# Kernel tuning notes

Measured on AMD Instinct MI355X. Metric: run time of the kernel, lower is better.

Reference implementation:

```python
import jax, jax.numpy as jnp
import numpy as np

NUM_CLASSES = 80
NUM_ANCHORS = 3
IN_H, IN_W = 608, 608
GRID_H, GRID_W = 76, 76
BATCH = 16
# anchors selected by anchor_mask [0,1,2] out of the 9 COCO anchors
MASKED_ANCHORS = np.array([[10.0, 13.0], [16.0, 30.0], [33.0, 23.0]], dtype=np.float32)


def setup_inputs() -> dict:
    key = jax.random.key(0)
    x = jax.random.normal(key, (BATCH, NUM_ANCHORS * (5 + NUM_CLASSES), GRID_H, GRID_W), dtype=jnp.float32)
    anchors = jnp.asarray(MASKED_ANCHORS)
    return {"x": x, "anchors": anchors}


def reference(x, anchors):
    """YOLOv3 detection-layer forward (decode path of Yolo.__cal_bounding_box).

    x: [N, A*(5+C), H, W] raw conv output; anchors: [A, 2] (w, h) in pixels.
    Returns decoded predictions [N, A*H*W, 5+C] with normalized xywh boxes,
    objectness and class probabilities.
    """
    N, _, H, W = x.shape
    A, C = NUM_ANCHORS, NUM_CLASSES
    x = x.reshape(N, A, 5 + C, H, W)  # [N, A, 5+C, H, W]

    px = jax.nn.sigmoid(x[:, :, 0])            # [N, A, H, W]
    py = jax.nn.sigmoid(x[:, :, 1])
    pw = x[:, :, 2]
    ph = x[:, :, 3]
    conf = jax.nn.sigmoid(x[:, :, 4])          # [N, A, H, W]
    prob = jax.nn.sigmoid(x[:, :, 5:])         # [N, A, C, H, W]

    gy, gx = jnp.meshgrid(jnp.arange(H, dtype=x.dtype), jnp.arange(W, dtype=x.dtype), indexing="ij")
    # grid-offset decode, normalized to [0, 1] (matches __cal_bounding_box)
    bx = (px + gx) / W
    by = (py + gy) / H
    aw = anchors[:, 0].reshape(1, A, 1, 1)
    ah = anchors[:, 1].reshape(1, A, 1, 1)
    bw = jnp.exp(pw) * aw / IN_W
    bh = jnp.exp(ph) * ah / IN_H

    bbox = jnp.stack([bx, by, bw, bh, conf], axis=-1)      # [N, A, H, W, 5]
    prob = jnp.transpose(prob, (0, 1, 3, 4, 2))            # [N, A, H, W, C]
    out = jnp.concatenate([bbox, prob], axis=-1)           # [N, A, H, W, 5+C]
    return out.reshape(N, A * H * W, 5 + C)
```

## Files before the change

### kernel.cpp

```cpp
#include <hip/hip_runtime.h>
#include <math.h>


#define NCH     85
#define SPATIAL 5776
#define GWID    76
#define TS      64
#define NTILES  91

__device__ __forceinline__ float fast_sigmoid(float v) {
    return __builtin_amdgcn_rcpf(1.0f + __expf(-v));
}

__device__ __forceinline__ void process4(float* __restrict__ tile,
                                         int c, int sl, int s0,
                                         float4 v, float aw, float ah) {
    float vv[4] = {v.x, v.y, v.z, v.w};
    if (c >= 4) {
        #pragma unroll
        for (int jj = 0; jj < 4; ++jj)
            tile[(sl + jj) * NCH + c] = fast_sigmoid(vv[jj]);
    } else if (c == 0) {
        #pragma unroll
        for (int jj = 0; jj < 4; ++jj) {
            const int sg = s0 + sl + jj;
            tile[(sl + jj) * NCH + c] =
                (fast_sigmoid(vv[jj]) + (float)(sg % GWID)) * (1.0f / GWID);
        }
    } else if (c == 1) {
        #pragma unroll
        for (int jj = 0; jj < 4; ++jj) {
            const int sg = s0 + sl + jj;
            tile[(sl + jj) * NCH + c] =
                (fast_sigmoid(vv[jj]) + (float)(sg / GWID)) * (1.0f / GWID);
        }
    } else if (c == 2) {
        #pragma unroll
        for (int jj = 0; jj < 4; ++jj)
            tile[(sl + jj) * NCH + c] = __expf(vv[jj]) * aw;
    } else {
        #pragma unroll
        for (int jj = 0; jj < 4; ++jj)
            tile[(sl + jj) * NCH + c] = __expf(vv[jj]) * ah;
    }
}

__global__ __launch_bounds__(256) void yolo_decode(
    const float* __restrict__ x,
    const float* __restrict__ anchors,
    float* __restrict__ out)
{
    __shared__ __align__(16) float tile[NCH * TS];

    const int na  = blockIdx.y;
    const int a   = na % 3;
    const int s0  = blockIdx.x * TS;
    const int t   = threadIdx.x;

    const float aw = anchors[a * 2 + 0] * (1.0f / 608.0f);
    const float ah = anchors[a * 2 + 1] * (1.0f / 608.0f);

    const float* in_base = x + (size_t)na * NCH * SPATIAL + s0;
    float* out_base = out + ((size_t)na * SPATIAL + s0) * NCH;

    if (s0 + TS <= SPATIAL) {
        const int sl    = (t & 15) << 2;
        const int cbase = t >> 4;
        const bool extra = (t < 80);

        const float* p = in_base + cbase * SPATIAL + sl;
        float4 v0 = *reinterpret_cast<const float4*>(p);
        float4 v1 = *reinterpret_cast<const float4*>(p + 16 * SPATIAL);
        float4 v2 = *reinterpret_cast<const float4*>(p + 32 * SPATIAL);
        float4 v3 = *reinterpret_cast<const float4*>(p + 48 * SPATIAL);
        float4 v4 = *reinterpret_cast<const float4*>(p + 64 * SPATIAL);
        float4 vt;
        int ct = 80 + cbase;
        if (extra)
            vt = *reinterpret_cast<const float4*>(in_base + ct * SPATIAL + sl);

        process4(tile, cbase +  0, sl, s0, v0, aw, ah);
        process4(tile, cbase + 16, sl, s0, v1, aw, ah);
        process4(tile, cbase + 32, sl, s0, v2, aw, ah);
        process4(tile, cbase + 48, sl, s0, v3, aw, ah);
        process4(tile, cbase + 64, sl, s0, v4, aw, ah);
        if (extra)
            process4(tile, ct, sl, s0, vt, aw, ah);

        __syncthreads();

        const int fb = t << 2;
        float4 o0 = *reinterpret_cast<const float4*>(&tile[fb]);
        float4 o1 = *reinterpret_cast<const float4*>(&tile[fb + 1024]);
        float4 o2 = *reinterpret_cast<const float4*>(&tile[fb + 2048]);
        float4 o3 = *reinterpret_cast<const float4*>(&tile[fb + 3072]);
        float4 o4 = *reinterpret_cast<const float4*>(&tile[fb + 4096]);
        *reinterpret_cast<float4*>(out_base + fb)        = o0;
        *reinterpret_cast<float4*>(out_base + fb + 1024) = o1;
        *reinterpret_cast<float4*>(out_base + fb + 2048) = o2;
        *reinterpret_cast<float4*>(out_base + fb + 3072) = o3;
        *reinterpret_cast<float4*>(out_base + fb + 4096) = o4;
        if (extra) {
            const int fbt = 5120 + (t << 2);
            float4 ot = *reinterpret_cast<const float4*>(&tile[fbt]);
            *reinterpret_cast<float4*>(out_base + fbt) = ot;
        }
    } else {
        const int rem = SPATIAL - s0;
        for (int idx = t; idx < NCH * (rem / 4); idx += 256) {
            const int c  = idx / (rem / 4);
            const int sl = (idx - c * (rem / 4)) << 2;
            const float4 v = *reinterpret_cast<const float4*>(
                in_base + c * SPATIAL + sl);
            process4(tile, c, sl, s0, v, aw, ah);
        }
        __syncthreads();
        const int nv4 = (NCH * rem) >> 2;
        for (int v = t; v < nv4; v += 256) {
            const float4 o = *reinterpret_cast<const float4*>(&tile[v << 2]);
            *reinterpret_cast<float4*>(out_base + (v << 2)) = o;
        }
    }
}

extern "C" void kernel_launch(void* const* d_in, const int* in_sizes, int n_in,
                              void* d_out, int out_size, void* d_ws, size_t ws_size,
                              hipStream_t stream) {
    const float* x       = (const float*)d_in[0];
    const float* anchors = (const float*)d_in[1];
    float* out           = (float*)d_out;

    dim3 grid(NTILES, 48);
    yolo_decode<<<grid, 256, 0, stream>>>(x, anchors, out);
}
```

Baseline: 168.7 us.

## Make blocks persistent over three tiles with register-prefetched next-tile loads

Each block now handles three consecutive tiles from a flattened 1D grid. It loads the next tile's inputs into registers while it processes and stores the current tile, so global reads overlap with transpose and store work. LDS barriers use inline s_waitcnt plus s_barrier, and the launch bounds request 5 blocks per SIMD. This costs more registers and fewer blocks, and the tail-tile path's indexing (idx>>2 with a 16-wide remainder) and an unused LOAD_FULL macro show some untidiness.

```diff
diff --git a/kernel.cpp b/kernel.cpp
--- a/kernel.cpp
+++ b/kernel.cpp
@@ -2,11 +2,14 @@
 #include <math.h>
 
 
-#define NCH     85
-#define SPATIAL 5776
-#define GWID    76
-#define TS      64
-#define NTILES  91
+#define NCH          85
+#define SPATIAL      5776
+#define GWID         76
+#define TS           64
+#define TILES_PER_NA 91
+#define TOTAL_TILES  (TILES_PER_NA * 48)
+#define NT           3
+#define NBLOCKS      (TOTAL_TILES / NT)
 
 __device__ __forceinline__ float fast_sigmoid(float v) {
     return __builtin_amdgcn_rcpf(1.0f + __expf(-v));
@@ -45,81 +48,132 @@
     }
 }
 
-__global__ __launch_bounds__(256) void yolo_decode(
+#define LOAD_FULL(tid, A0, A1, A2, A3, A4, A5)                                 \
+    do {                                                                       \
+        const int na_ = (tid) / TILES_PER_NA;                                  \
+        const int j_  = (tid) - na_ * TILES_PER_NA;                            \
+        const float* p_ = x + (size_t)na_ * NCH * SPATIAL + j_ * TS            \
+                            + cbase * SPATIAL + sl;                            \
+        A0 = *reinterpret_cast<const float4*>(p_);                             \
+        A1 = *reinterpret_cast<const float4*>(p_ + 16 * SPATIAL);              \
+        A2 = *reinterpret_cast<const float4*>(p_ + 32 * SPATIAL);              \
+        A3 = *reinterpret_cast<const float4*>(p_ + 48 * SPATIAL);              \
+        A4 = *reinterpret_cast<const float4*>(p_ + 64 * SPATIAL);              \
+        if (extra)                                                             \
+            A5 = *reinterpret_cast<const float4*>(p_ + (80 - cbase + cbase + 64 + 16 - 64) * SPATIAL + (80 + cbase - cbase - 16) * SPATIAL); \
+    } while (0)
+
+#define LDS_BAR() asm volatile("s_waitcnt lgkmcnt(0)\n\ts_barrier" ::: "memory")
+
+__global__ __launch_bounds__(256, 5) void yolo_decode(
     const float* __restrict__ x,
     const float* __restrict__ anchors,
     float* __restrict__ out)
 {
     __shared__ __align__(16) float tile[NCH * TS];
 
-    const int na  = blockIdx.y;
-    const int a   = na % 3;
-    const int s0  = blockIdx.x * TS;
-    const int t   = threadIdx.x;
+    const int t     = threadIdx.x;
+    const int sl    = (t & 15) << 2;
+    const int cbase = t >> 4;
+    const bool extra = (t < 80);
 
-    const float aw = anchors[a * 2 + 0] * (1.0f / 608.0f);
-    const float ah = anchors[a * 2 + 1] * (1.0f / 608.0f);
+    int tid = blockIdx.x * NT;
 
-    const float* in_base = x + (size_t)na * NCH * SPATIAL + s0;
-    float* out_base = out + ((size_t)na * SPATIAL + s0) * NCH;
+    float4 R0, R1, R2, R3, R4, R5;
+    float4 N0, N1, N2, N3, N4, N5;
 
-    if (s0 + TS <= SPATIAL) {
-        const int sl    = (t & 15) << 2;
-        const int cbase = t >> 4;
-        const bool extra = (t < 80);
+    bool pf_cur = ((tid % TILES_PER_NA) != TILES_PER_NA - 1);
+    if (pf_cur) {
+        const int na_ = tid / TILES_PER_NA;
+        const int j_  = tid - na_ * TILES_PER_NA;
+        const float* p_ = x + (size_t)na_ * NCH * SPATIAL + j_ * TS
+                            + cbase * SPATIAL + sl;
+        R0 = *reinterpret_cast<const float4*>(p_);
+        R1 = *reinterpret_cast<const float4*>(p_ + 16 * SPATIAL);
+        R2 = *reinterpret_cast<const float4*>(p_ + 32 * SPATIAL);
+        R3 = *reinterpret_cast<const float4*>(p_ + 48 * SPATIAL);
+        R4 = *reinterpret_cast<const float4*>(p_ + 64 * SPATIAL);
+        if (extra)
+            R5 = *reinterpret_cast<const float4*>(p_ + (80 - cbase) * SPATIAL
+                                                     + cbase * SPATIAL);
+    }
 
-        const float* p = in_base + cbase * SPATIAL + sl;
-        float4 v0 = *reinterpret_cast<const float4*>(p);
-        float4 v1 = *reinterpret_cast<const float4*>(p + 16 * SPATIAL);
-        float4 v2 = *reinterpret_cast<const float4*>(p + 32 * SPATIAL);
-        float4 v3 = *reinterpret_cast<const float4*>(p + 48 * SPATIAL);
-        float4 v4 = *reinterpret_cast<const float4*>(p + 64 * SPATIAL);
-        float4 vt;
-        int ct = 80 + cbase;
-        if (extra)
-            vt = *reinterpret_cast<const float4*>(in_base + ct * SPATIAL + sl);
+    #pragma unroll 1
+    for (int i = 0; i < NT; ++i, ++tid) {
+        const int na = tid / TILES_PER_NA;
+        const int j  = tid - na * TILES_PER_NA;
+        const int s0 = j * TS;
+        const int a  = na % 3;
+        const float aw = anchors[2 * a]     * (1.0f / 608.0f);
+        const float ah = anchors[2 * a + 1] * (1.0f / 608.0f);
+        const float* in_base = x + (size_t)na * NCH * SPATIAL + s0;
+        float* out_base = out + ((size_t)na * SPATIAL + s0) * NCH;
 
-        process4(tile, cbase +  0, sl, s0, v0, aw, ah);
-        process4(tile, cbase + 16, sl, s0, v1, aw, ah);
-        process4(tile, cbase + 32, sl, s0, v2, aw, ah);
-        process4(tile, cbase + 48, sl, s0, v3, aw, ah);
-        process4(tile, cbase + 64, sl, s0, v4, aw, ah);
-        if (extra)
-            process4(tile, ct, sl, s0, vt, aw, ah);
+        const bool pf_next = (i + 1 < NT) &&
+                             (((tid + 1) % TILES_PER_NA) != TILES_PER_NA - 1);
+        if (pf_next) {
+            const int na_ = (tid + 1) / TILES_PER_NA;
+            const int j_  = (tid + 1) - na_ * TILES_PER_NA;
+            const float* p_ = x + (size_t)na_ * NCH * SPATIAL + j_ * TS
+                                + cbase * SPATIAL + sl;
+            N0 = *reinterpret_cast<const float4*>(p_);
+            N1 = *reinterpret_cast<const float4*>(p_ + 16 * SPATIAL);
+            N2 = *reinterpret_cast<const float4*>(p_ + 32 * SPATIAL);
+            N3 = *reinterpret_cast<const float4*>(p_ + 48 * SPATIAL);
+            N4 = *reinterpret_cast<const float4*>(p_ + 64 * SPATIAL);
+            if (extra)
+                N5 = *reinterpret_cast<const float4*>(p_ + 80 * SPATIAL);
+        }
 
-        __syncthreads();
+        if (pf_cur) {
+            process4(tile, cbase +  0, sl, s0, R0, aw, ah);
+            process4(tile, cbase + 16, sl, s0, R1, aw, ah);
+            process4(tile, cbase + 32, sl, s0, R2, aw, ah);
+            process4(tile, cbase + 48, sl, s0, R3, aw, ah);
+            process4(tile, cbase + 64, sl, s0, R4, aw, ah);
+            if (extra)
+                process4(tile, cbase + 80, sl, s0, R5, aw, ah);
 
-        const int fb = t << 2;
-        float4 o0 = *reinterpret_cast<const float4*>(&tile[fb]);
-        float4 o1 = *reinterpret_cast<const float4*>(&tile[fb + 1024]);
-        float4 o2 = *reinterpret_cast<const float4*>(&tile[fb + 2048]);
-        float4 o3 = *reinterpret_cast<const float4*>(&tile[fb + 3072]);
-        float4 o4 = *reinterpret_cast<const float4*>(&tile[fb + 4096]);
-        *reinterpret_cast<float4*>(out_base + fb)        = o0;
-        *reinterpret_cast<float4*>(out_base + fb + 1024) = o1;
-        *reinterpret_cast<float4*>(out_base + fb + 2048) = o2;
-        *reinterpret_cast<float4*>(out_base + fb + 3072) = o3;
-        *reinterpret_cast<float4*>(out_base + fb + 4096) = o4;
-        if (extra) {
-            const int fbt = 5120 + (t << 2);
-            float4 ot = *reinterpret_cast<const float4*>(&tile[fbt]);
-            *reinterpret_cast<float4*>(out_base + fbt) = ot;
+            LDS_BAR();
+
+            const int fb = t << 2;
+            float4 o0 = *reinterpret_cast<const float4*>(&tile[fb]);
+            float4 o1 = *reinterpret_cast<const float4*>(&tile[fb + 1024]);
+            float4 o2 = *reinterpret_cast<const float4*>(&tile[fb + 2048]);
+            float4 o3 = *reinterpret_cast<const float4*>(&tile[fb + 3072]);
+            float4 o4 = *reinterpret_cast<const float4*>(&tile[fb + 4096]);
+            *reinterpret_cast<float4*>(out_base + fb)        = o0;
+            *reinterpret_cast<float4*>(out_base + fb + 1024) = o1;
+            *reinterpret_cast<float4*>(out_base + fb + 2048) = o2;
+            *reinterpret_cast<float4*>(out_base + fb + 3072) = o3;
+            *reinterpret_cast<float4*>(out_base + fb + 4096) = o4;
+            if (extra) {
+                const int fbt = 5120 + (t << 2);
+                float4 ot = *reinterpret_cast<const float4*>(&tile[fbt]);
+                *reinterpret_cast<float4*>(out_base + fbt) = ot;
+            }
+
+            LDS_BAR();
+        } else {
+            const int rem = SPATIAL - s0;
+            for (int idx = t; idx < NCH * (rem / 4); idx += 256) {
+                const int c   = idx >> 2;
+                const int slx = (idx & 3) << 2;
+                const float4 v = *reinterpret_cast<const float4*>(
+                    in_base + c * SPATIAL + slx);
+                process4(tile, c, slx, s0, v, aw, ah);
+            }
+            __syncthreads();
+            const int nv4 = (NCH * rem) >> 2;
+            for (int v = t; v < nv4; v += 256) {
+                const float4 o = *reinterpret_cast<const float4*>(&tile[v << 2]);
+                *reinterpret_cast<float4*>(out_base + (v << 2)) = o;
+            }
+            __syncthreads();
         }
-    } else {
-        const int rem = SPATIAL - s0;
-        for (int idx = t; idx < NCH * (rem / 4); idx += 256) {
-            const int c  = idx / (rem / 4);
-            const int sl = (idx - c * (rem / 4)) << 2;
-            const float4 v = *reinterpret_cast<const float4*>(
-                in_base + c * SPATIAL + sl);
-            process4(tile, c, sl, s0, v, aw, ah);
-        }
-        __syncthreads();
-        const int nv4 = (NCH * rem) >> 2;
-        for (int v = t; v < nv4; v += 256) {
-            const float4 o = *reinterpret_cast<const float4*>(&tile[v << 2]);
-            *reinterpret_cast<float4*>(out_base + (v << 2)) = o;
-        }
+
+        R0 = N0; R1 = N1; R2 = N2; R3 = N3; R4 = N4; R5 = N5;
+        pf_cur = pf_next;
     }
 }
 
@@ -130,6 +184,5 @@
     const float* anchors = (const float*)d_in[1];
     float* out           = (float*)d_out;
 
-    dim3 grid(NTILES, 48);
-    yolo_decode<<<grid, 256, 0, stream>>>(x, anchors, out);
+    yolo_decode<<<dim3(NBLOCKS), 256, 0, stream>>>(x, anchors, out);
 }
```

After: 175.1 us. 3.8% more time.
